# Optimization experiments

Measured on AMD Instinct MI355X. Metric: run time of the kernel, lower is better.

The kernel has to match this reference:

```python
import jax, jax.numpy as jnp
import numpy as np

N = 100_000   # nodes
E = 640_000   # edges
H = 128       # hidden_dim
L = 4         # num_layers
C = 2         # num_classes
G = 128       # graphs in batch

def setup_inputs() -> dict:
    key = jax.random.key(0)
    ks = jax.random.split(key, 8)
    x = jax.random.randint(ks[0], (N, 1), 0, 2)
    edge_index = jax.random.randint(ks[1], (2, E), 0, N)
    batch = jnp.sort(jax.random.randint(ks[2], (N,), 0, G))
    embed = jax.random.normal(ks[3], (2, H), jnp.float32)
    Ws = jax.random.normal(ks[4], (L, H, H), jnp.float32) * (1.0 / np.sqrt(H))
    bs = jnp.zeros((L, H), jnp.float32)
    W_out = jax.random.normal(ks[5], (H, C), jnp.float32) * (1.0 / np.sqrt(H))
    b_out = jnp.zeros((C,), jnp.float32)
    return dict(x=x, edge_index=edge_index, batch=batch, embed=embed,
                Ws=Ws, bs=bs, W_out=W_out, b_out=b_out)

def reference(x, edge_index, batch, embed, Ws, bs, W_out, b_out):
    src, dst = edge_index[0], edge_index[1]
    # symmetric GCN normalization with self-loops (PyG GCNConv default)
    deg = jax.ops.segment_sum(jnp.ones(E, jnp.float32), dst, num_segments=N) + 1.0
    dinv = jax.lax.rsqrt(deg)
    enorm = (dinv[src] * dinv[dst])[:, None]   # per-edge norm
    snorm = (dinv * dinv)[:, None]             # self-loop norm

    h = embed[x[:, 0]]                          # [N, H] embedding lookup
    n_layers = Ws.shape[0]
    for l in range(n_layers):
        t = h @ Ws[l]                           # linear transform [N, H]
        agg = jax.ops.segment_sum(t[src] * enorm, dst, num_segments=N) \
              + t * snorm + bs[l]
        h = jax.nn.relu(agg) if l < n_layers - 1 else agg

    # global mean pool over graph ids
    counts = jax.ops.segment_sum(jnp.ones(N, jnp.float32), batch, num_segments=G)
    pooled = jax.ops.segment_sum(h, batch, num_segments=G) \
             / jnp.maximum(counts, 1.0)[:, None]   # [G, H]
    return pooled @ W_out + b_out                  # [G, C]
```

## Files before the change

### kernel.cpp

```cpp
#include <hip/hip_runtime.h>

typedef __attribute__((ext_vector_type(8))) short bf16x8;
typedef __attribute__((ext_vector_type(4))) float f32x4;
typedef __attribute__((ext_vector_type(2))) float f32x2;

__device__ inline unsigned short bf16_rtn(float f) {
  unsigned u = __float_as_uint(f);
  unsigned r = u + 0x7fffu + ((u >> 16) & 1u);
  return (unsigned short)(r >> 16);
}

__device__ inline void split_bf16(float f, unsigned short& hi, unsigned short& lo) {
  hi = bf16_rtn(f);
  float fh = __uint_as_float((unsigned)hi << 16);
  lo = bf16_rtn(f - fh);
}

__device__ inline unsigned char f_to_fp8(float f) {
  int r = __builtin_amdgcn_cvt_pk_fp8_f32(f, f, 0, false);
  return (unsigned char)(r & 0xff);
}
__device__ inline f32x2 fp8x2_to_f(unsigned short v) {
  return __builtin_amdgcn_cvt_pk_f32_fp8((int)v, false);
}


__global__ void k_hist(const int* __restrict__ dst, int* __restrict__ deg, int E) {
  int e = blockIdx.x * 256 + threadIdx.x;
  if (e < E) atomicAdd(&deg[dst[e]], 1);
}

__global__ void k_scan1(const int* __restrict__ deg, int* __restrict__ rowptr,
                        int* __restrict__ bsum, float* __restrict__ dinv, int N) {
  __shared__ int s[256];
  int t = threadIdx.x;
  int i = blockIdx.x * 256 + t;
  int v = (i < N) ? deg[i] : 0;
  if (i < N) dinv[i] = rsqrtf((float)v + 1.0f);
  s[t] = v;
  __syncthreads();
  for (int off = 1; off < 256; off <<= 1) {
    int u = (t >= off) ? s[t - off] : 0;
    __syncthreads();
    s[t] += u;
    __syncthreads();
  }
  if (i < N) rowptr[i] = s[t] - v;
  if (t == 255) bsum[blockIdx.x] = s[255];
}

__global__ void k_scan2(const int* __restrict__ bsum, int* __restrict__ boff, int nb) {
  __shared__ int s[512];
  int t = threadIdx.x;
  int v = (t < nb) ? bsum[t] : 0;
  s[t] = v;
  __syncthreads();
  for (int off = 1; off < 512; off <<= 1) {
    int u = (t >= off) ? s[t - off] : 0;
    __syncthreads();
    s[t] += u;
    __syncthreads();
  }
  boff[t] = s[t] - v;
}

__global__ void k_scan3(int* __restrict__ rowptr, const int* __restrict__ boff,
                        int* __restrict__ cursor, int N, int E) {
  int i = blockIdx.x * 256 + threadIdx.x;
  if (i < N) {
    int r = rowptr[i] + boff[i >> 8];
    rowptr[i] = r;
    cursor[i] = r;
  }
  if (i == 0) rowptr[N] = E;
}

__global__ void k_scatter(const int* __restrict__ src, const int* __restrict__ dst,
                          const float* __restrict__ dinv, int* __restrict__ cursor,
                          int* __restrict__ esrc, float* __restrict__ ew, int E) {
  int e = blockIdx.x * 256 + threadIdx.x;
  if (e >= E) return;
  int s = src[e], d = dst[e];
  float w = dinv[s] * dinv[d];
  int pos = atomicAdd(&cursor[d], 1);
  esrc[pos] = s;
  ew[pos] = w;
}

__global__ void k_prepWT(const float* __restrict__ Ws, const float* __restrict__ embed,
                         unsigned short* __restrict__ wphi,
                         unsigned short* __restrict__ wplo,
                         float* __restrict__ T) {
  int l = blockIdx.x;
  if (l == 3) {
    int t = threadIdx.x;
    int r = t >> 7, c = t & 127;
    float acc = 0.f;
    for (int k = 0; k < 128; ++k)
      acc += embed[r * 128 + k] * Ws[k * 128 + c];
    T[r * 128 + c] = acc;
    return;
  }
  const float* W = Ws + (size_t)(l + 1) * 128 * 128;
  unsigned short* dh = wphi + (size_t)l * 16384;
  unsigned short* dl = wplo + (size_t)l * 16384;
  for (int idx = threadIdx.x; idx < 16384; idx += 256) {
    int j = idx & 7;
    int lane = (idx >> 3) & 63;
    int c = (idx >> 9) & 3;
    int ct = idx >> 11;
    int k = c * 32 + ((lane >> 4) * 8) + j;
    int n = ct * 16 + (lane & 15);
    unsigned short hi, lo;
    split_bf16(W[k * 128 + n], hi, lo);
    dh[idx] = hi;
    dl[idx] = lo;
  }
}

__global__ void k_bounds(const int* __restrict__ batch, int* __restrict__ gstart,
                         int* __restrict__ gend, int N) {
  int i = blockIdx.x * 256 + threadIdx.x;
  if (i >= N) return;
  int g = batch[i];
  if (i == 0 || batch[i - 1] != g) gstart[g] = i;
  if (i == N - 1 || batch[i + 1] != g) gend[g] = i + 1;
}

__device__ inline void gather_node(const unsigned char* __restrict__ tin,
                                   const int* __restrict__ esrc,
                                   const float* __restrict__ ew,
                                   int r0, int deg, int lane,
                                   float& a0, float& a1) {
  int dcap = deg < 64 ? deg : 64;
  int sl = 0; float wl = 0.f;
  if (lane < dcap) { sl = esrc[r0 + lane]; wl = ew[r0 + lane]; }
  a0 = 0.f; a1 = 0.f;
  int e = 0;
  for (; e + 4 <= dcap; e += 4) {
    int s0 = __shfl(sl, e, 64),     s1 = __shfl(sl, e + 1, 64);
    int s2 = __shfl(sl, e + 2, 64), s3 = __shfl(sl, e + 3, 64);
    float w0 = __shfl(wl, e, 64),     w1 = __shfl(wl, e + 1, 64);
    float w2 = __shfl(wl, e + 2, 64), w3 = __shfl(wl, e + 3, 64);
    unsigned short p0 = *(const unsigned short*)(tin + (size_t)s0 * 128 + 2 * lane);
    unsigned short p1 = *(const unsigned short*)(tin + (size_t)s1 * 128 + 2 * lane);
    unsigned short p2 = *(const unsigned short*)(tin + (size_t)s2 * 128 + 2 * lane);
    unsigned short p3 = *(const unsigned short*)(tin + (size_t)s3 * 128 + 2 * lane);
    f32x2 v0 = fp8x2_to_f(p0), v1 = fp8x2_to_f(p1);
    f32x2 v2 = fp8x2_to_f(p2), v3 = fp8x2_to_f(p3);
    a0 += w0 * v0.x + w1 * v1.x + w2 * v2.x + w3 * v3.x;
    a1 += w0 * v0.y + w1 * v1.y + w2 * v2.y + w3 * v3.y;
  }
  for (; e < dcap; ++e) {
    int s = __shfl(sl, e, 64);
    float w = __shfl(wl, e, 64);
    unsigned short p = *(const unsigned short*)(tin + (size_t)s * 128 + 2 * lane);
    f32x2 v = fp8x2_to_f(p);
    a0 += w * v.x;
    a1 += w * v.y;
  }
  for (int ee = r0 + 64; ee < r0 + deg; ++ee) {
    int s = esrc[ee];
    float w = ew[ee];
    unsigned short p = *(const unsigned short*)(tin + (size_t)s * 128 + 2 * lane);
    f32x2 v = fp8x2_to_f(p);
    a0 += w * v.x;
    a1 += w * v.y;
  }
}

__device__ inline void gemm_tile8(const unsigned short* hT,
                                  const unsigned short* __restrict__ wphi,
                                  const unsigned short* __restrict__ wplo,
                                  unsigned char* __restrict__ tout, int i0, int N) {
  int ct = threadIdx.x >> 6;
  int lane = threadIdx.x & 63;
  int q = lane >> 4;
  int m = lane & 15;
  const bf16x8* bh_base = (const bf16x8*)wphi;
  const bf16x8* bl_base = (const bf16x8*)wplo;

  f32x4 acc0 = (f32x4){0.f, 0.f, 0.f, 0.f};
  f32x4 acc1 = (f32x4){0.f, 0.f, 0.f, 0.f};

  #pragma unroll
  for (int c = 0; c < 4; ++c) {
    bf16x8 a0 = *(const bf16x8*)(hT + (m) * 136 + c * 32 + q * 8);
    bf16x8 a1 = *(const bf16x8*)(hT + (16 + m) * 136 + c * 32 + q * 8);
    bf16x8 bh = bh_base[(ct * 4 + c) * 64 + lane];
    bf16x8 bl = bl_base[(ct * 4 + c) * 64 + lane];
    acc0 = __builtin_amdgcn_mfma_f32_16x16x32_bf16(a0, bh, acc0, 0, 0, 0);
    acc0 = __builtin_amdgcn_mfma_f32_16x16x32_bf16(a0, bl, acc0, 0, 0, 0);
    acc1 = __builtin_amdgcn_mfma_f32_16x16x32_bf16(a1, bh, acc1, 0, 0, 0);
    acc1 = __builtin_amdgcn_mfma_f32_16x16x32_bf16(a1, bl, acc1, 0, 0, 0);
  }

  #pragma unroll
  for (int r = 0; r < 4; ++r) {
    int row0 = i0 + q * 4 + r;
    int row1 = row0 + 16;
    if (row0 < N) tout[(size_t)row0 * 128 + ct * 16 + m] = f_to_fp8(acc0[r]);
    if (row1 < N) tout[(size_t)row1 * 128 + ct * 16 + m] = f_to_fp8(acc1[r]);
  }
}

__global__ __launch_bounds__(512)
void k_l1_gemm(const int* __restrict__ x, const int* __restrict__ rowptr,
               const int* __restrict__ esrc, const float* __restrict__ ew,
               const float* __restrict__ dinv, const float* __restrict__ T,
               const float* __restrict__ b0,
               const unsigned short* __restrict__ wphi,
               const unsigned short* __restrict__ wplo,
               unsigned char* __restrict__ tout, int N) {
  __shared__ unsigned short hT[32 * 136];
  int wave = threadIdx.x >> 6;
  int lane = threadIdx.x & 63;
  int i0 = blockIdx.x * 32;

  for (int j = wave * 4; j < wave * 4 + 4; ++j) {
    int i = i0 + j;
    if (i >= N) break;
    int r0 = rowptr[i], r1 = rowptr[i + 1];
    float c0 = 0.f, c1 = 0.f;
    for (int e = r0 + lane; e < r1; e += 64) {
      float w = ew[e];
      int s = esrc[e];
      if (x[s]) c1 += w; else c0 += w;
    }
    for (int mm = 32; mm >= 1; mm >>= 1) {
      c0 += __shfl_xor(c0, mm, 64);
      c1 += __shfl_xor(c1, mm, 64);
    }
    float di = dinv[i];
    float sn = di * di;
    if (x[i]) c1 += sn; else c0 += sn;
    float v0 = fmaxf(c0 * T[2 * lane]     + c1 * T[128 + 2 * lane]     + b0[2 * lane],     0.f);
    float v1 = fmaxf(c0 * T[2 * lane + 1] + c1 * T[128 + 2 * lane + 1] + b0[2 * lane + 1], 0.f);
    *(unsigned*)&hT[j * 136 + 2 * lane] = (unsigned)bf16_rtn(v0) | ((unsigned)bf16_rtn(v1) << 16);
  }
  __syncthreads();
  gemm_tile8(hT, wphi, wplo, tout, i0, N);
}

__global__ __launch_bounds__(512)
void k_agg_gemm(const unsigned char* __restrict__ tin,
                const int* __restrict__ rowptr,
                const int* __restrict__ esrc, const float* __restrict__ ew,
                const float* __restrict__ dinv, const float* __restrict__ bvec,
                const unsigned short* __restrict__ wphi,
                const unsigned short* __restrict__ wplo,
                unsigned char* __restrict__ tout, int N) {
  __shared__ unsigned short hT[32 * 136];
  int wave = threadIdx.x >> 6;
  int lane = threadIdx.x & 63;
  int i0 = blockIdx.x * 32;
  float2 bv = *(const float2*)(bvec + 2 * lane);

  for (int j = wave * 4; j < wave * 4 + 4; ++j) {
    int i = i0 + j;
    if (i >= N) break;
    int r0 = rowptr[i], r1 = rowptr[i + 1];
    float a0, a1;
    gather_node(tin, esrc, ew, r0, r1 - r0, lane, a0, a1);
    float di = dinv[i];
    float sn = di * di;
    unsigned short ps = *(const unsigned short*)(tin + (size_t)i * 128 + 2 * lane);
    f32x2 sv = fp8x2_to_f(ps);
    a0 += sn * sv.x;
    a1 += sn * sv.y;
    float v0 = fmaxf(a0 + bv.x, 0.f);
    float v1 = fmaxf(a1 + bv.y, 0.f);
    *(unsigned*)&hT[j * 136 + 2 * lane] = (unsigned)bf16_rtn(v0) | ((unsigned)bf16_rtn(v1) << 16);
  }
  __syncthreads();
  gemm_tile8(hT, wphi, wplo, tout, i0, N);
}

__global__ __launch_bounds__(512)
void k_agg_pool(const unsigned char* __restrict__ tin,
                const int* __restrict__ rowptr,
                const int* __restrict__ esrc, const float* __restrict__ ew,
                const float* __restrict__ dinv, const float* __restrict__ bvec,
                const int* __restrict__ batch,
                float* __restrict__ pooled, int N) {
  int wave = threadIdx.x >> 6;
  int lane = threadIdx.x & 63;
  int i0w = blockIdx.x * 32 + wave * 4;
  if (i0w >= N) return;
  float2 bv = *(const float2*)(bvec + 2 * lane);

  float acc0 = 0.f, acc1 = 0.f;
  int curg = batch[i0w];
  for (int n = 0; n < 4; ++n) {
    int i = i0w + n;
    if (i >= N) break;
    int r0 = rowptr[i], r1 = rowptr[i + 1];
    float a0, a1;
    gather_node(tin, esrc, ew, r0, r1 - r0, lane, a0, a1);
    float di = dinv[i];
    float sn = di * di;
    unsigned short ps = *(const unsigned short*)(tin + (size_t)i * 128 + 2 * lane);
    f32x2 sv = fp8x2_to_f(ps);
    a0 += sn * sv.x + bv.x;
    a1 += sn * sv.y + bv.y;
    int g = batch[i];
    if (g != curg) {
      atomicAdd(&pooled[curg * 128 + 2 * lane], acc0);
      atomicAdd(&pooled[curg * 128 + 2 * lane + 1], acc1);
      acc0 = 0.f; acc1 = 0.f;
      curg = g;
    }
    acc0 += a0;
    acc1 += a1;
  }
  atomicAdd(&pooled[curg * 128 + 2 * lane], acc0);
  atomicAdd(&pooled[curg * 128 + 2 * lane + 1], acc1);
}

__global__ void k_out(const float* __restrict__ pooled, const int* __restrict__ gstart,
                      const int* __restrict__ gend, const float* __restrict__ W_out,
                      const float* __restrict__ b_out, float* __restrict__ out, int G) {
  __shared__ float sp[128];
  int g = blockIdx.x;
  int j = threadIdx.x;
  float cnt = (float)(gend[g] - gstart[g]);
  sp[j] = pooled[g * 128 + j] / fmaxf(cnt, 1.f);
  __syncthreads();
  if (j < 2) {
    float o = b_out[j];
    for (int k = 0; k < 128; ++k)
      o += sp[k] * W_out[k * 2 + j];
    out[g * 2 + j] = o;
  }
}

extern "C" void kernel_launch(void* const* d_in, const int* in_sizes, int n_in,
                              void* d_out, int out_size, void* d_ws, size_t ws_size,
                              hipStream_t stream) {
  const int*   x     = (const int*)d_in[0];
  const int*   ei    = (const int*)d_in[1];
  const int*   batch = (const int*)d_in[2];
  const float* embed = (const float*)d_in[3];
  const float* Ws    = (const float*)d_in[4];
  const float* bs    = (const float*)d_in[5];
  const float* W_out = (const float*)d_in[6];
  const float* b_out = (const float*)d_in[7];
  float* out = (float*)d_out;

  int N = in_sizes[2];
  int E = in_sizes[1] / 2;
  int G = out_size / 2;

  const int* src = ei;
  const int* dst = ei + E;

  char* w = (char*)d_ws;
  auto alloc = [&](size_t bytes) {
    char* p = w;
    w += (bytes + 255) & ~(size_t)255;
    return p;
  };
  int*   deg    = (int*)  alloc((size_t)N * 4);
  float* dinv   = (float*)alloc((size_t)N * 4);
  int*   rowptr = (int*)  alloc((size_t)(N + 1) * 4);
  int*   cursor = (int*)  alloc((size_t)N * 4);
  int*   bsum   = (int*)  alloc(512 * 4);
  int*   boff   = (int*)  alloc(512 * 4);
  int*   gstart = (int*)  alloc((size_t)G * 4);
  int*   gend   = (int*)  alloc((size_t)G * 4);
  float* pooled = (float*)alloc((size_t)G * 128 * 4);
  float* T      = (float*)alloc(256 * 4);
  unsigned short* wphi = (unsigned short*)alloc((size_t)3 * 16384 * 2);
  unsigned short* wplo = (unsigned short*)alloc((size_t)3 * 16384 * 2);
  int*   esrc   = (int*)  alloc((size_t)E * 4);
  float* eww    = (float*)alloc((size_t)E * 4);
  unsigned char* t_a = (unsigned char*)alloc((size_t)N * 128);
  unsigned char* t_b = (unsigned char*)alloc((size_t)N * 128);

  int nbN = (N + 255) / 256;
  int nbE = (E + 255) / 256;
  int ntile = (N + 31) / 32;

  size_t gzero = (size_t)((char*)pooled - (char*)gstart) + (size_t)G * 128 * 4;
  hipMemsetAsync(deg, 0, (size_t)N * 4, stream);
  hipMemsetAsync(gstart, 0, gzero, stream);

  k_hist<<<nbE, 256, 0, stream>>>(dst, deg, E);
  k_scan1<<<nbN, 256, 0, stream>>>(deg, rowptr, bsum, dinv, N);
  k_scan2<<<1, 512, 0, stream>>>(bsum, boff, nbN);
  k_scan3<<<nbN, 256, 0, stream>>>(rowptr, boff, cursor, N, E);
  k_scatter<<<nbE, 256, 0, stream>>>(src, dst, dinv, cursor, esrc, eww, E);
  k_prepWT<<<4, 256, 0, stream>>>(Ws, embed, wphi, wplo, T);
  k_bounds<<<nbN, 256, 0, stream>>>(batch, gstart, gend, N);

  k_l1_gemm<<<ntile, 512, 0, stream>>>(x, rowptr, esrc, eww, dinv, T, bs,
                                       wphi, wplo, t_a, N);
  k_agg_gemm<<<ntile, 512, 0, stream>>>(t_a, rowptr, esrc, eww, dinv, bs + 128,
                                        wphi + 16384, wplo + 16384, t_b, N);
  k_agg_gemm<<<ntile, 512, 0, stream>>>(t_b, rowptr, esrc, eww, dinv, bs + 256,
                                        wphi + 32768, wplo + 32768, t_a, N);
  k_agg_pool<<<ntile, 512, 0, stream>>>(t_a, rowptr, esrc, eww, dinv, bs + 384,
                                        batch, pooled, N);
  k_out<<<G, 128, 0, stream>>>(pooled, gstart, gend, W_out, b_out, out, G);
}
```

Baseline: 350.5 us.

## Split fused aggregate+GEMM kernels into separate aggregate, GEMM and pool kernels

Replaces the fused per-tile aggregate-then-GEMM kernels with a standalone one-wave-per-node aggregation kernel that writes bf16 hidden states to global memory, then a separate MFMA GEMM kernel that reads them back. The final layer's pooling is also split into its own kernel. The goal is to decouple the irregular gather from the GEMM so each stage gets its own launch shape and occupancy. The cost is an extra bf16 N×128 round trip through global memory per layer, plus additional launches. The k_gemm tail rows read h past N without bounds checks.

```diff
diff --git a/kernel.cpp b/kernel.cpp
--- a/kernel.cpp
+++ b/kernel.cpp
@@ -14,6 +14,10 @@
   hi = bf16_rtn(f);
   float fh = __uint_as_float((unsigned)hi << 16);
   lo = bf16_rtn(f - fh);
+}
+
+__device__ inline float bf16_to_f(unsigned short v) {
+  return __uint_as_float((unsigned)v << 16);
 }
 
 __device__ inline unsigned char f_to_fp8(float f) {
@@ -169,6 +173,98 @@
   }
 }
 
+__global__ void k_agg(const unsigned char* __restrict__ tin,
+                      const int* __restrict__ rowptr,
+                      const int* __restrict__ esrc, const float* __restrict__ ew,
+                      const float* __restrict__ dinv, const float* __restrict__ bvec,
+                      unsigned short* __restrict__ h, int N, int dorelu) {
+  int i = (blockIdx.x * blockDim.x + threadIdx.x) >> 6;
+  int lane = threadIdx.x & 63;
+  if (i >= N) return;
+  int r0 = rowptr[i], r1 = rowptr[i + 1];
+  float a0, a1;
+  gather_node(tin, esrc, ew, r0, r1 - r0, lane, a0, a1);
+  float di = dinv[i];
+  float sn = di * di;
+  unsigned short ps = *(const unsigned short*)(tin + (size_t)i * 128 + 2 * lane);
+  f32x2 sv = fp8x2_to_f(ps);
+  float2 bv = *(const float2*)(bvec + 2 * lane);
+  a0 += sn * sv.x + bv.x;
+  a1 += sn * sv.y + bv.y;
+  if (dorelu) { a0 = fmaxf(a0, 0.f); a1 = fmaxf(a1, 0.f); }
+  *(unsigned*)(h + (size_t)i * 128 + 2 * lane) =
+      (unsigned)bf16_rtn(a0) | ((unsigned)bf16_rtn(a1) << 16);
+}
+
+__global__ void k_gemm(const unsigned short* __restrict__ h,
+                       const unsigned short* __restrict__ wphi,
+                       const unsigned short* __restrict__ wplo,
+                       unsigned char* __restrict__ tout, int N) {
+  int wave = threadIdx.x >> 6;
+  int lane = threadIdx.x & 63;
+  int r0 = (blockIdx.x * 4 + wave) * 32;
+  if (r0 >= N) return;
+  int q = lane >> 4;
+  int m = lane & 15;
+  const bf16x8* bh_base = (const bf16x8*)wphi;
+  const bf16x8* bl_base = (const bf16x8*)wplo;
+
+  f32x4 acc[2][8];
+  #pragma unroll
+  for (int tt = 0; tt < 2; ++tt)
+    #pragma unroll
+    for (int ct = 0; ct < 8; ++ct)
+      acc[tt][ct] = (f32x4){0.f, 0.f, 0.f, 0.f};
+
+  for (int c = 0; c < 4; ++c) {
+    bf16x8 a0 = *(const bf16x8*)(h + (size_t)(r0 + m) * 128 + c * 32 + q * 8);
+    bf16x8 a1 = *(const bf16x8*)(h + (size_t)(r0 + 16 + m) * 128 + c * 32 + q * 8);
+    #pragma unroll
+    for (int ct = 0; ct < 8; ++ct) {
+      bf16x8 bh = bh_base[(ct * 4 + c) * 64 + lane];
+      bf16x8 bl = bl_base[(ct * 4 + c) * 64 + lane];
+      acc[0][ct] = __builtin_amdgcn_mfma_f32_16x16x32_bf16(a0, bh, acc[0][ct], 0, 0, 0);
+      acc[0][ct] = __builtin_amdgcn_mfma_f32_16x16x32_bf16(a0, bl, acc[0][ct], 0, 0, 0);
+      acc[1][ct] = __builtin_amdgcn_mfma_f32_16x16x32_bf16(a1, bh, acc[1][ct], 0, 0, 0);
+      acc[1][ct] = __builtin_amdgcn_mfma_f32_16x16x32_bf16(a1, bl, acc[1][ct], 0, 0, 0);
+    }
+  }
+
+  #pragma unroll
+  for (int tt = 0; tt < 2; ++tt)
+    #pragma unroll
+    for (int ct = 0; ct < 8; ++ct)
+      #pragma unroll
+      for (int r = 0; r < 4; ++r) {
+        int row = r0 + tt * 16 + q * 4 + r;
+        if (row < N)
+          tout[(size_t)row * 128 + ct * 16 + m] = f_to_fp8(acc[tt][ct][r]);
+      }
+}
+
+__global__ void k_pool_partial(const unsigned short* __restrict__ h,
+                               const int* __restrict__ batch,
+                               float* __restrict__ pooled, int N) {
+  int c = threadIdx.x & 127;
+  int half = threadIdx.x >> 7;
+  int rbeg = blockIdx.x * 64 + half * 32;
+  int rend = rbeg + 32;
+  if (rend > N) rend = N;
+  if (rbeg >= N) return;
+  float acc = 0.f;
+  int curg = batch[rbeg];
+  for (int i = rbeg; i < rend; ++i) {
+    int g = batch[i];
+    if (g != curg) {
+      atomicAdd(&pooled[curg * 128 + c], acc);
+      acc = 0.f;
+      curg = g;
+    }
+    acc += bf16_to_f(h[(size_t)i * 128 + c]);
+  }
+  atomicAdd(&pooled[curg * 128 + c], acc);
+}
+
 __device__ inline void gemm_tile8(const unsigned short* hT,
                                   const unsigned short* __restrict__ wphi,
                                   const unsigned short* __restrict__ wplo,
@@ -242,81 +338,6 @@
   gemm_tile8(hT, wphi, wplo, tout, i0, N);
 }
 
-__global__ __launch_bounds__(512)
-void k_agg_gemm(const unsigned char* __restrict__ tin,
-                const int* __restrict__ rowptr,
-                const int* __restrict__ esrc, const float* __restrict__ ew,
-                const float* __restrict__ dinv, const float* __restrict__ bvec,
-                const unsigned short* __restrict__ wphi,
-                const unsigned short* __restrict__ wplo,
-                unsigned char* __restrict__ tout, int N) {
-  __shared__ unsigned short hT[32 * 136];
-  int wave = threadIdx.x >> 6;
-  int lane = threadIdx.x & 63;
-  int i0 = blockIdx.x * 32;
-  float2 bv = *(const float2*)(bvec + 2 * lane);
-
-  for (int j = wave * 4; j < wave * 4 + 4; ++j) {
-    int i = i0 + j;
-    if (i >= N) break;
-    int r0 = rowptr[i], r1 = rowptr[i + 1];
-    float a0, a1;
-    gather_node(tin, esrc, ew, r0, r1 - r0, lane, a0, a1);
-    float di = dinv[i];
-    float sn = di * di;
-    unsigned short ps = *(const unsigned short*)(tin + (size_t)i * 128 + 2 * lane);
-    f32x2 sv = fp8x2_to_f(ps);
-    a0 += sn * sv.x;
-    a1 += sn * sv.y;
-    float v0 = fmaxf(a0 + bv.x, 0.f);
-    float v1 = fmaxf(a1 + bv.y, 0.f);
-    *(unsigned*)&hT[j * 136 + 2 * lane] = (unsigned)bf16_rtn(v0) | ((unsigned)bf16_rtn(v1) << 16);
-  }
-  __syncthreads();
-  gemm_tile8(hT, wphi, wplo, tout, i0, N);
-}
-
-__global__ __launch_bounds__(512)
-void k_agg_pool(const unsigned char* __restrict__ tin,
-                const int* __restrict__ rowptr,
-                const int* __restrict__ esrc, const float* __restrict__ ew,
-                const float* __restrict__ dinv, const float* __restrict__ bvec,
-                const int* __restrict__ batch,
-                float* __restrict__ pooled, int N) {
-  int wave = threadIdx.x >> 6;
-  int lane = threadIdx.x & 63;
-  int i0w = blockIdx.x * 32 + wave * 4;
-  if (i0w >= N) return;
-  float2 bv = *(const float2*)(bvec + 2 * lane);
-
-  float acc0 = 0.f, acc1 = 0.f;
-  int curg = batch[i0w];
-  for (int n = 0; n < 4; ++n) {
-    int i = i0w + n;
-    if (i >= N) break;
-    int r0 = rowptr[i], r1 = rowptr[i + 1];
-    float a0, a1;
-    gather_node(tin, esrc, ew, r0, r1 - r0, lane, a0, a1);
-    float di = dinv[i];
-    float sn = di * di;
-    unsigned short ps = *(const unsigned short*)(tin + (size_t)i * 128 + 2 * lane);
-    f32x2 sv = fp8x2_to_f(ps);
-    a0 += sn * sv.x + bv.x;
-    a1 += sn * sv.y + bv.y;
-    int g = batch[i];
-    if (g != curg) {
-      atomicAdd(&pooled[curg * 128 + 2 * lane], acc0);
-      atomicAdd(&pooled[curg * 128 + 2 * lane + 1], acc1);
-      acc0 = 0.f; acc1 = 0.f;
-      curg = g;
-    }
-    acc0 += a0;
-    acc1 += a1;
-  }
-  atomicAdd(&pooled[curg * 128 + 2 * lane], acc0);
-  atomicAdd(&pooled[curg * 128 + 2 * lane + 1], acc1);
-}
-
 __global__ void k_out(const float* __restrict__ pooled, const int* __restrict__ gstart,
                       const int* __restrict__ gend, const float* __restrict__ W_out,
                       const float* __restrict__ b_out, float* __restrict__ out, int G) {
@@ -374,12 +395,14 @@
   unsigned short* wplo = (unsigned short*)alloc((size_t)3 * 16384 * 2);
   int*   esrc   = (int*)  alloc((size_t)E * 4);
   float* eww    = (float*)alloc((size_t)E * 4);
+  unsigned short* h = (unsigned short*)alloc((size_t)N * 128 * 2);
   unsigned char* t_a = (unsigned char*)alloc((size_t)N * 128);
   unsigned char* t_b = (unsigned char*)alloc((size_t)N * 128);
 
   int nbN = (N + 255) / 256;
   int nbE = (E + 255) / 256;
   int ntile = (N + 31) / 32;
+  int nwb = (N + 3) / 4;
 
   size_t gzero = (size_t)((char*)pooled - (char*)gstart) + (size_t)G * 128 * 4;
   hipMemsetAsync(deg, 0, (size_t)N * 4, stream);
@@ -395,11 +418,11 @@
 
   k_l1_gemm<<<ntile, 512, 0, stream>>>(x, rowptr, esrc, eww, dinv, T, bs,
                                        wphi, wplo, t_a, N);
-  k_agg_gemm<<<ntile, 512, 0, stream>>>(t_a, rowptr, esrc, eww, dinv, bs + 128,
-                                        wphi + 16384, wplo + 16384, t_b, N);
-  k_agg_gemm<<<ntile, 512, 0, stream>>>(t_b, rowptr, esrc, eww, dinv, bs + 256,
-                                        wphi + 32768, wplo + 32768, t_a, N);
-  k_agg_pool<<<ntile, 512, 0, stream>>>(t_a, rowptr, esrc, eww, dinv, bs + 384,
-                                        batch, pooled, N);
+  k_agg<<<nwb, 256, 0, stream>>>(t_a, rowptr, esrc, eww, dinv, bs + 128, h, N, 1);
+  k_gemm<<<(N / 32 + 3) / 4 + 1, 256, 0, stream>>>(h, wphi + 16384, wplo + 16384, t_b, N);
+  k_agg<<<nwb, 256, 0, stream>>>(t_b, rowptr, esrc, eww, dinv, bs + 256, h, N, 1);
+  k_gemm<<<(N / 32 + 3) / 4 + 1, 256, 0, stream>>>(h, wphi + 32768, wplo + 32768, t_a, N);
+  k_agg<<<nwb, 256, 0, stream>>>(t_a, rowptr, esrc, eww, dinv, bs + 384, h, N, 0);
+  k_pool_partial<<<(N + 63) / 64, 256, 0, stream>>>(h, batch, pooled, N);
   k_out<<<G, 128, 0, stream>>>(pooled, gstart, gend, W_out, b_out, out, G);
 }
```

After: 358.0 us. +2.1%, slower.
